# Kernel tuning notes

Hardware: AMD Instinct MI355X
Metric: run time of the kernel (lower is better)

Reference implementation:

```python
import jax, jax.numpy as jnp
import numpy as np

B, N, E = 128, 2048, 32768   # events, nodes per history graph, temporal edges per graph
C, TC, H = 4, 4, 2           # channels, time_channels, heads (hardcoded in source)
DH = C // H
L = 2                        # num_layers


def setup_inputs() -> dict:
    key = jax.random.key(0)
    ks = jax.random.split(key, 16)
    return {
        "x": jax.random.normal(ks[0], (B, N, C), jnp.float32),
        "edge_index": jax.random.randint(ks[1], (B, 2, E), 0, N),
        "edge_time": jax.random.uniform(ks[2], (B, E), jnp.float32),
        "timestamp": jax.random.uniform(ks[3], (B,), jnp.float32),
        "src_index": jax.random.randint(ks[4], (B,), 0, N),
        "dst_index": jax.random.randint(ks[5], (B,), 0, N),
        "time_w": jax.random.normal(ks[6], (TC,), jnp.float32),
        "time_b": jax.random.normal(ks[7], (TC,), jnp.float32),
        "Wq": jax.random.normal(ks[8], (L, C, C), jnp.float32) / np.sqrt(C).astype(np.float32),
        "Wk": jax.random.normal(ks[9], (L, C + TC, C), jnp.float32) / np.sqrt(C + TC).astype(np.float32),
        "Wv": jax.random.normal(ks[10], (L, C + TC, C), jnp.float32) / np.sqrt(C + TC).astype(np.float32),
        "Wo": jax.random.normal(ks[11], (L, C, C), jnp.float32) / np.sqrt(C).astype(np.float32),
        "bo": jnp.zeros((L, C), jnp.float32),
        "W_lin": jax.random.normal(ks[12], (2 * C + TC, 2), jnp.float32) / np.sqrt(2 * C + TC).astype(np.float32),
        "b_lin": jnp.zeros((2,), jnp.float32),
    }


def _time_enc(t, w, b):
    # TimeEncoder: cos(t * w + b)  (Bochner-style functional time encoding)
    return jnp.cos(t[..., None] * w + b)


def _encode(x, src, dst, phi, Wq, Wk, Wv, Wo, bo):
    # seg id per edge: (batch, dst node) -> flat segment for segment softmax
    seg = (jnp.arange(B, dtype=dst.dtype)[:, None] * N + dst).reshape(-1)  # [B*E]
    h = x
    for l in range(L):
        h_src = jnp.take_along_axis(h, src[:, :, None], axis=1)            # [B,E,C] gather source feats
        msg = jnp.concatenate([h_src, phi], axis=-1)                       # [B,E,C+TC]
        q = (h @ Wq[l]).reshape(B, N, C)                                   # [B,N,C]
        k = (msg @ Wk[l]).reshape(B, E, H, DH)
        v = (msg @ Wv[l]).reshape(B, E, H, DH)
        q_e = jnp.take_along_axis(q, dst[:, :, None], axis=1).reshape(B, E, H, DH)
        logits = (q_e * k).sum(-1) / np.float32(np.sqrt(DH))               # [B,E,H]
        lf = logits.reshape(B * E, H)
        m = jax.ops.segment_max(lf, seg, num_segments=B * N)               # stable softmax max
        p = jnp.exp(lf - m[seg])
        s = jax.ops.segment_sum(p, seg, num_segments=B * N)
        agg = jax.ops.segment_sum(p[:, :, None] * v.reshape(B * E, H, DH), seg, num_segments=B * N)
        attn = (agg / jnp.where(s == 0, 1.0, s)[:, :, None]).reshape(B, N, C)
        h = jax.nn.relu(h + attn @ Wo[l] + bo[l])                          # residual + out-proj + relu
    return h


def reference(x, edge_index, edge_time, timestamp, src_index, dst_index,
              time_w, time_b, Wq, Wk, Wv, Wo, bo, W_lin, b_lin):
    src, dst = edge_index[:, 0, :], edge_index[:, 1, :]
    dt = timestamp[:, None] - edge_time                                    # [B,E] time deltas vs query time
    phi = _time_enc(dt, time_w, time_b)                                    # [B,E,TC]
    h = _encode(x, src, dst, phi, Wq, Wk, Wv, Wo, bo)                      # [B,N,C]
    bidx = jnp.arange(B)
    src_x = h[bidx, src_index]                                             # [B,C]
    dst_x = h[bidx, dst_index]                                             # [B,C]
    time_x = _time_enc(timestamp, time_w, time_b)                          # [B,TC]
    feats = jnp.concatenate([src_x, dst_x, time_x], axis=-1)               # [B,12]
    return feats @ W_lin + b_lin                                           # [B,2]
```

## Files before the change

kernel.cpp:

```cpp
#include <hip/hip_runtime.h>
#include <hip/hip_fp16.h>

namespace {

constexpr int B = 128, N = 2048, E = 32768;
constexpr int LOG2N = 11, LOG2E = 15;
constexpr int QE = 8192;

constexpr size_t OFF_H0  = 0;
constexpr size_t OFF_H1  = 4u * 1024 * 1024;
constexpr size_t OFF_SRT = 8u * 1024 * 1024;
constexpr size_t OFF_SEG = 24u * 1024 * 1024;

__global__ __launch_bounds__(1024) void sort_kernel(const int* __restrict__ edge_index,
                                                    const float* __restrict__ edge_time,
                                                    const float* __restrict__ timestamp,
                                                    unsigned* __restrict__ sorted,
                                                    unsigned* __restrict__ seg) {
  __shared__ int      cnt[N];
  __shared__ int      partial[1024];
  __shared__ unsigned rec[QE];
  int blk = blockIdx.x, b = blk >> 2, q = blk & 3, t = threadIdx.x;
  const int* src_arr = edge_index + ((size_t)(2 * b) << LOG2E) + q * QE;
  const int* dst_arr = edge_index + ((size_t)(2 * b + 1) << LOG2E) + q * QE;
  const float* et    = edge_time + ((size_t)b << LOG2E) + q * QE;
  float ts = timestamp[b];

  cnt[t] = 0; cnt[t + 1024] = 0;
  __syncthreads();

  for (int e = t; e < QE; e += 1024) atomicAdd(&cnt[dst_arr[e]], 1);
  __syncthreads();

  int i0 = 2 * t, i1 = 2 * t + 1;
  int l0 = cnt[i0], l1 = cnt[i1], sum = l0 + l1;
  partial[t] = sum;
  __syncthreads();
  for (int d = 1; d < 1024; d <<= 1) {
    int v = (t >= d) ? partial[t - d] : 0;
    __syncthreads();
    partial[t] += v;
    __syncthreads();
  }
  int run = partial[t] - sum;
  int run2 = run + l0;
  unsigned* sg = seg + (size_t)blk * N;
  sg[i0] = (unsigned)run  | ((unsigned)l0 << 16);
  sg[i1] = (unsigned)run2 | ((unsigned)l1 << 16);
  cnt[i0] = run;
  cnt[i1] = run2;
  __syncthreads();

  for (int e = t; e < QE; e += 1024) {
    int dst = dst_arr[e], src = src_arr[e];
    float dt = ts - et[e];
    unsigned hd = (unsigned)__half_as_ushort(__float2half(dt));
    int pos = atomicAdd(&cnt[dst], 1);
    rec[pos] = (unsigned)src | (hd << 16);
  }
  __syncthreads();

  const uint4* rec4 = (const uint4*)rec;
  uint4* out4 = (uint4*)(sorted + ((size_t)blk << 13));
#pragma unroll
  for (int i = t; i < QE / 4; i += 1024) out4[i] = rec4[i];
}

__global__ __launch_bounds__(256) void layer_kernel(const float4* __restrict__ h_in,
                                                    float4* __restrict__ h_out,
                                                    const unsigned* __restrict__ seg,
                                                    const unsigned* __restrict__ sorted,
                                                    const float* __restrict__ tw,
                                                    const float* __restrict__ tb,
                                                    const float* __restrict__ Wq,
                                                    const float* __restrict__ Wk,
                                                    const float* __restrict__ Wv,
                                                    const float* __restrict__ Wo,
                                                    const float* __restrict__ bo) {
  __shared__ float4 lh[N];
  int blk = blockIdx.x, b = blk >> 3, oct = blk & 7, t = threadIdx.x;

  const float4* hb = h_in + ((size_t)b << LOG2N);
#pragma unroll
  for (int j = 0; j < 8; j++) {
    int idx = j * 256 + t;
    lh[idx] = hb[idx];
  }

  float twf[4], tbf[4], bof[4], wq[16], wof[16], wk[32], wv[32];
#pragma unroll
  for (int j = 0; j < 4; j++) { twf[j] = tw[j]; tbf[j] = tb[j]; bof[j] = bo[j]; }
#pragma unroll
  for (int j = 0; j < 16; j++) { wq[j] = Wq[j]; wof[j] = Wo[j]; }
#pragma unroll
  for (int j = 0; j < 32; j++) { wk[j] = Wk[j]; wv[j] = Wv[j]; }
  __syncthreads();

  int n = (oct << 8) + t;
  float4 hn = lh[n];
  float q0 = hn.x * wq[0] + hn.y * wq[4] + hn.z * wq[8]  + hn.w * wq[12];
  float q1 = hn.x * wq[1] + hn.y * wq[5] + hn.z * wq[9]  + hn.w * wq[13];
  float q2 = hn.x * wq[2] + hn.y * wq[6] + hn.z * wq[10] + hn.w * wq[14];
  float q3 = hn.x * wq[3] + hn.y * wq[7] + hn.z * wq[11] + hn.w * wq[15];
  const float RS2 = 0.70710678118654752f;
  float u0[8], u1[8];
#pragma unroll
  for (int j = 0; j < 8; j++) {
    u0[j] = RS2 * (q0 * wk[j * 4 + 0] + q1 * wk[j * 4 + 1]);
    u1[j] = RS2 * (q2 * wk[j * 4 + 2] + q3 * wk[j * 4 + 3]);
  }

  float m0 = -INFINITY, m1 = -INFINITY;
  float s0 = 0.f, s1 = 0.f, a00 = 0.f, a01 = 0.f, a10 = 0.f, a11 = 0.f;

#pragma unroll
  for (int q = 0; q < 4; ++q) {
    int qblk = (b << 2) + q;
    unsigned sd = seg[(size_t)qblk * N + n];
    int beg = (int)(sd & 0xFFFFu);
    int deg = (int)(sd >> 16);
    const unsigned* srt = sorted + ((size_t)qblk << 13) + beg;
    unsigned rc = (deg > 0) ? srt[0] : 0u;
    for (int j = 0; j < deg; ++j) {
      unsigned rc_next = (j + 1 < deg) ? srt[j + 1] : 0u;
      int src = (int)(rc & 0xFFFFu);
      float dt = __half2float(__ushort_as_half((unsigned short)(rc >> 16)));
      float4 hs = lh[src];
      float p0c = __cosf(dt * twf[0] + tbf[0]);
      float p1c = __cosf(dt * twf[1] + tbf[1]);
      float p2c = __cosf(dt * twf[2] + tbf[2]);
      float p3c = __cosf(dt * twf[3] + tbf[3]);
      float l0 = u0[0] * hs.x + u0[1] * hs.y + u0[2] * hs.z + u0[3] * hs.w
               + u0[4] * p0c + u0[5] * p1c + u0[6] * p2c + u0[7] * p3c;
      float l1 = u1[0] * hs.x + u1[1] * hs.y + u1[2] * hs.z + u1[3] * hs.w
               + u1[4] * p0c + u1[5] * p1c + u1[6] * p2c + u1[7] * p3c;
      float v0 = wv[0] * hs.x + wv[4] * hs.y + wv[8]  * hs.z + wv[12] * hs.w
               + wv[16] * p0c + wv[20] * p1c + wv[24] * p2c + wv[28] * p3c;
      float v1 = wv[1] * hs.x + wv[5] * hs.y + wv[9]  * hs.z + wv[13] * hs.w
               + wv[17] * p0c + wv[21] * p1c + wv[25] * p2c + wv[29] * p3c;
      float v2 = wv[2] * hs.x + wv[6] * hs.y + wv[10] * hs.z + wv[14] * hs.w
               + wv[18] * p0c + wv[22] * p1c + wv[26] * p2c + wv[30] * p3c;
      float v3 = wv[3] * hs.x + wv[7] * hs.y + wv[11] * hs.z + wv[15] * hs.w
               + wv[19] * p0c + wv[23] * p1c + wv[27] * p2c + wv[31] * p3c;
      float nm0 = fmaxf(m0, l0);
      float sc0 = __expf(m0 - nm0);
      float p0  = __expf(l0 - nm0);
      s0 = s0 * sc0 + p0; a00 = a00 * sc0 + p0 * v0; a01 = a01 * sc0 + p0 * v1; m0 = nm0;
      float nm1 = fmaxf(m1, l1);
      float sc1 = __expf(m1 - nm1);
      float p1  = __expf(l1 - nm1);
      s1 = s1 * sc1 + p1; a10 = a10 * sc1 + p1 * v2; a11 = a11 * sc1 + p1 * v3; m1 = nm1;
      rc = rc_next;
    }
  }
  float d0 = (s0 == 0.f) ? 1.f : s0;
  float d1 = (s1 == 0.f) ? 1.f : s1;
  float at0 = a00 / d0, at1 = a01 / d0, at2 = a10 / d1, at3 = a11 / d1;
  float o0 = bof[0] + at0 * wof[0] + at1 * wof[4] + at2 * wof[8]  + at3 * wof[12];
  float o1 = bof[1] + at0 * wof[1] + at1 * wof[5] + at2 * wof[9]  + at3 * wof[13];
  float o2 = bof[2] + at0 * wof[2] + at1 * wof[6] + at2 * wof[10] + at3 * wof[14];
  float o3 = bof[3] + at0 * wof[3] + at1 * wof[7] + at2 * wof[11] + at3 * wof[15];
  h_out[((size_t)b << LOG2N) + n] =
      make_float4(fmaxf(hn.x + o0, 0.f), fmaxf(hn.y + o1, 0.f),
                  fmaxf(hn.z + o2, 0.f), fmaxf(hn.w + o3, 0.f));
}

__global__ void final_kernel(const float4* __restrict__ h,
                             const int* __restrict__ src_index, const int* __restrict__ dst_index,
                             const float* __restrict__ timestamp,
                             const float* __restrict__ tw,
                             const float* __restrict__ tb,
                             const float* __restrict__ W_lin,
                             const float* __restrict__ b_lin,
                             float* __restrict__ out) {
  int b = threadIdx.x;
  if (b >= B) return;
  float4 sx = h[(((size_t)b) << LOG2N) + src_index[b]];
  float4 dx = h[(((size_t)b) << LOG2N) + dst_index[b]];
  float ts = timestamp[b];
  float f[12];
  f[0] = sx.x; f[1] = sx.y; f[2] = sx.z; f[3] = sx.w;
  f[4] = dx.x; f[5] = dx.y; f[6] = dx.z; f[7] = dx.w;
#pragma unroll
  for (int j = 0; j < 4; j++) f[8 + j] = __cosf(ts * tw[j] + tb[j]);
#pragma unroll
  for (int c = 0; c < 2; c++) {
    float o = b_lin[c];
#pragma unroll
    for (int j = 0; j < 12; j++) o += f[j] * W_lin[j * 2 + c];
    out[b * 2 + c] = o;
  }
}

}

extern "C" void kernel_launch(void* const* d_in, const int* in_sizes, int n_in,
                              void* d_out, int out_size, void* d_ws, size_t ws_size,
                              hipStream_t stream) {
  (void)in_sizes; (void)n_in; (void)out_size; (void)ws_size;
  const float* x         = (const float*)d_in[0];
  const int*   edge_idx  = (const int*)d_in[1];
  const float* edge_time = (const float*)d_in[2];
  const float* timestamp = (const float*)d_in[3];
  const int*   src_index = (const int*)d_in[4];
  const int*   dst_index = (const int*)d_in[5];
  const float* time_w    = (const float*)d_in[6];
  const float* time_b    = (const float*)d_in[7];
  const float* Wq        = (const float*)d_in[8];
  const float* Wk        = (const float*)d_in[9];
  const float* Wv        = (const float*)d_in[10];
  const float* Wo        = (const float*)d_in[11];
  const float* bo        = (const float*)d_in[12];
  const float* W_lin     = (const float*)d_in[13];
  const float* b_lin     = (const float*)d_in[14];

  char* ws = (char*)d_ws;
  float4*   h0     = (float4*)(ws + OFF_H0);
  float4*   h1     = (float4*)(ws + OFF_H1);
  unsigned* sorted = (unsigned*)(ws + OFF_SRT);
  unsigned* seg    = (unsigned*)(ws + OFF_SEG);

  sort_kernel<<<4 * B, 1024, 0, stream>>>(edge_idx, edge_time, timestamp, sorted, seg);

  layer_kernel<<<8 * B, 256, 0, stream>>>((const float4*)x, h1, seg, sorted,
                                          time_w, time_b,
                                          Wq + 0 * 16, Wk + 0 * 32, Wv + 0 * 32,
                                          Wo + 0 * 16, bo + 0 * 4);
  layer_kernel<<<8 * B, 256, 0, stream>>>(h1, h0, seg, sorted,
                                          time_w, time_b,
                                          Wq + 1 * 16, Wk + 1 * 32, Wv + 1 * 32,
                                          Wo + 1 * 16, bo + 1 * 4);

  final_kernel<<<1, 128, 0, stream>>>(h0, src_index, dst_index, timestamp, time_w, time_b,
                                      W_lin, b_lin, (float*)d_out);
}
```

Baseline: 195.8 us.

## Pad per-node edge lists to multiples of four and process edges in uint4 chunks

The sort kernel now pads each destination node's record segment to a multiple of four, so every segment is 16-byte aligned and the sorted buffer stride grows. The layer kernel loads four packed edge records per uint4 and processes them as a block, using a single online-softmax rescale per chunk instead of one per edge. This targets per-edge scalar global loads and the serial exp/max dependency chain. In exchange it adds wasted work on padded lanes, a larger sorted buffer, and more register pressure from the unrolled four-edge body.

```diff
diff --git a/kernel.cpp b/kernel.cpp
--- a/kernel.cpp
+++ b/kernel.cpp
@@ -6,11 +6,13 @@
 constexpr int B = 128, N = 2048, E = 32768;
 constexpr int LOG2N = 11, LOG2E = 15;
 constexpr int QE = 8192;
+constexpr int RECCAP = 14336;
+constexpr int SSTR = 16384;
 
 constexpr size_t OFF_H0  = 0;
 constexpr size_t OFF_H1  = 4u * 1024 * 1024;
 constexpr size_t OFF_SRT = 8u * 1024 * 1024;
-constexpr size_t OFF_SEG = 24u * 1024 * 1024;
+constexpr size_t OFF_SEG = 40u * 1024 * 1024;
 
 __global__ __launch_bounds__(1024) void sort_kernel(const int* __restrict__ edge_index,
                                                     const float* __restrict__ edge_time,
@@ -19,7 +21,8 @@
                                                     unsigned* __restrict__ seg) {
   __shared__ int      cnt[N];
   __shared__ int      partial[1024];
-  __shared__ unsigned rec[QE];
+  __shared__ int      tot_s;
+  __shared__ unsigned rec[RECCAP];
   int blk = blockIdx.x, b = blk >> 2, q = blk & 3, t = threadIdx.x;
   const int* src_arr = edge_index + ((size_t)(2 * b) << LOG2E) + q * QE;
   const int* dst_arr = edge_index + ((size_t)(2 * b + 1) << LOG2E) + q * QE;
@@ -33,7 +36,9 @@
   __syncthreads();
 
   int i0 = 2 * t, i1 = 2 * t + 1;
-  int l0 = cnt[i0], l1 = cnt[i1], sum = l0 + l1;
+  int d0 = cnt[i0], d1 = cnt[i1];
+  int w0 = (d0 + 3) & ~3, w1 = (d1 + 3) & ~3;
+  int sum = w0 + w1;
   partial[t] = sum;
   __syncthreads();
   for (int d = 1; d < 1024; d <<= 1) {
@@ -43,10 +48,11 @@
     __syncthreads();
   }
   int run = partial[t] - sum;
-  int run2 = run + l0;
+  int run2 = run + w0;
+  if (t == 1023) tot_s = partial[t];
   unsigned* sg = seg + (size_t)blk * N;
-  sg[i0] = (unsigned)run  | ((unsigned)l0 << 16);
-  sg[i1] = (unsigned)run2 | ((unsigned)l1 << 16);
+  sg[i0] = (unsigned)run  | ((unsigned)d0 << 16);
+  sg[i1] = (unsigned)run2 | ((unsigned)d1 << 16);
   cnt[i0] = run;
   cnt[i1] = run2;
   __syncthreads();
@@ -60,10 +66,10 @@
   }
   __syncthreads();
 
+  int tot4 = tot_s >> 2;
   const uint4* rec4 = (const uint4*)rec;
-  uint4* out4 = (uint4*)(sorted + ((size_t)blk << 13));
-#pragma unroll
-  for (int i = t; i < QE / 4; i += 1024) out4[i] = rec4[i];
+  uint4* out4 = (uint4*)(sorted + (size_t)blk * SSTR);
+  for (int i = t; i < tot4; i += 1024) out4[i] = rec4[i];
 }
 
 __global__ __launch_bounds__(256) void layer_kernel(const float4* __restrict__ h_in,
@@ -110,47 +116,80 @@
     u1[j] = RS2 * (q2 * wk[j * 4 + 2] + q3 * wk[j * 4 + 3]);
   }
 
-  float m0 = -INFINITY, m1 = -INFINITY;
-  float s0 = 0.f, s1 = 0.f, a00 = 0.f, a01 = 0.f, a10 = 0.f, a11 = 0.f;
-
+  int begq[4], degq[4];
+  const uint4* sp[4];
 #pragma unroll
   for (int q = 0; q < 4; ++q) {
     int qblk = (b << 2) + q;
     unsigned sd = seg[(size_t)qblk * N + n];
-    int beg = (int)(sd & 0xFFFFu);
-    int deg = (int)(sd >> 16);
-    const unsigned* srt = sorted + ((size_t)qblk << 13) + beg;
-    unsigned rc = (deg > 0) ? srt[0] : 0u;
-    for (int j = 0; j < deg; ++j) {
-      unsigned rc_next = (j + 1 < deg) ? srt[j + 1] : 0u;
-      int src = (int)(rc & 0xFFFFu);
-      float dt = __half2float(__ushort_as_half((unsigned short)(rc >> 16)));
-      float4 hs = lh[src];
-      float p0c = __cosf(dt * twf[0] + tbf[0]);
-      float p1c = __cosf(dt * twf[1] + tbf[1]);
-      float p2c = __cosf(dt * twf[2] + tbf[2]);
-      float p3c = __cosf(dt * twf[3] + tbf[3]);
-      float l0 = u0[0] * hs.x + u0[1] * hs.y + u0[2] * hs.z + u0[3] * hs.w
-               + u0[4] * p0c + u0[5] * p1c + u0[6] * p2c + u0[7] * p3c;
-      float l1 = u1[0] * hs.x + u1[1] * hs.y + u1[2] * hs.z + u1[3] * hs.w
-               + u1[4] * p0c + u1[5] * p1c + u1[6] * p2c + u1[7] * p3c;
-      float v0 = wv[0] * hs.x + wv[4] * hs.y + wv[8]  * hs.z + wv[12] * hs.w
+    begq[q] = (int)(sd & 0xFFFFu);
+    degq[q] = (int)(sd >> 16);
+    sp[q] = (const uint4*)(sorted + (size_t)qblk * SSTR + begq[q]);
+  }
+  uint4 pf[4];
+#pragma unroll
+  for (int q = 0; q < 4; ++q)
+    pf[q] = (degq[q] > 0) ? sp[q][0] : make_uint4(0, 0, 0, 0);
+
+  float m0 = -INFINITY, m1 = -INFINITY;
+  float s0 = 0.f, s1 = 0.f, a00 = 0.f, a01 = 0.f, a10 = 0.f, a11 = 0.f;
+
+#pragma unroll
+  for (int q = 0; q < 4; ++q) {
+    int dg = degq[q];
+    if (dg <= 0) continue;
+    int nch = (dg + 3) >> 2;
+    uint4 cur = pf[q];
+    for (int c = 0; c < nch; ++c) {
+      uint4 nxt = (c + 1 < nch) ? sp[q][c + 1] : make_uint4(0, 0, 0, 0);
+      unsigned rcs[4] = {cur.x, cur.y, cur.z, cur.w};
+      int jb = c << 2;
+      float l0e[4], l1e[4], v0e[4], v1e[4], v2e[4], v3e[4];
+#pragma unroll
+      for (int i = 0; i < 4; ++i) {
+        bool valid = (jb + i) < dg;
+        unsigned rcv = valid ? rcs[i] : 0u;
+        int src = (int)(rcv & 0x7FFu);
+        float dt = __half2float(__ushort_as_half((unsigned short)(rcv >> 16)));
+        float4 hs = lh[src];
+        float p0c = __cosf(dt * twf[0] + tbf[0]);
+        float p1c = __cosf(dt * twf[1] + tbf[1]);
+        float p2c = __cosf(dt * twf[2] + tbf[2]);
+        float p3c = __cosf(dt * twf[3] + tbf[3]);
+        float l0 = u0[0] * hs.x + u0[1] * hs.y + u0[2] * hs.z + u0[3] * hs.w
+                 + u0[4] * p0c + u0[5] * p1c + u0[6] * p2c + u0[7] * p3c;
+        float l1 = u1[0] * hs.x + u1[1] * hs.y + u1[2] * hs.z + u1[3] * hs.w
+                 + u1[4] * p0c + u1[5] * p1c + u1[6] * p2c + u1[7] * p3c;
+        l0e[i] = valid ? l0 : -INFINITY;
+        l1e[i] = valid ? l1 : -INFINITY;
+        v0e[i] = wv[0] * hs.x + wv[4] * hs.y + wv[8]  * hs.z + wv[12] * hs.w
                + wv[16] * p0c + wv[20] * p1c + wv[24] * p2c + wv[28] * p3c;
-      float v1 = wv[1] * hs.x + wv[5] * hs.y + wv[9]  * hs.z + wv[13] * hs.w
+        v1e[i] = wv[1] * hs.x + wv[5] * hs.y + wv[9]  * hs.z + wv[13] * hs.w
                + wv[17] * p0c + wv[21] * p1c + wv[25] * p2c + wv[29] * p3c;
-      float v2 = wv[2] * hs.x + wv[6] * hs.y + wv[10] * hs.z + wv[14] * hs.w
+        v2e[i] = wv[2] * hs.x + wv[6] * hs.y + wv[10] * hs.z + wv[14] * hs.w
                + wv[18] * p0c + wv[22] * p1c + wv[26] * p2c + wv[30] * p3c;
-      float v3 = wv[3] * hs.x + wv[7] * hs.y + wv[11] * hs.z + wv[15] * hs.w
+        v3e[i] = wv[3] * hs.x + wv[7] * hs.y + wv[11] * hs.z + wv[15] * hs.w
                + wv[19] * p0c + wv[23] * p1c + wv[27] * p2c + wv[31] * p3c;
-      float nm0 = fmaxf(m0, l0);
+      }
+      float lx0 = fmaxf(fmaxf(l0e[0], l0e[1]), fmaxf(l0e[2], l0e[3]));
+      float nm0 = fmaxf(m0, lx0);
       float sc0 = __expf(m0 - nm0);
-      float p0  = __expf(l0 - nm0);
-      s0 = s0 * sc0 + p0; a00 = a00 * sc0 + p0 * v0; a01 = a01 * sc0 + p0 * v1; m0 = nm0;
-      float nm1 = fmaxf(m1, l1);
+      float pe0 = __expf(l0e[0] - nm0), pe1 = __expf(l0e[1] - nm0);
+      float pe2 = __expf(l0e[2] - nm0), pe3 = __expf(l0e[3] - nm0);
+      s0  = s0  * sc0 + (pe0 + pe1 + pe2 + pe3);
+      a00 = a00 * sc0 + (pe0 * v0e[0] + pe1 * v0e[1] + pe2 * v0e[2] + pe3 * v0e[3]);
+      a01 = a01 * sc0 + (pe0 * v1e[0] + pe1 * v1e[1] + pe2 * v1e[2] + pe3 * v1e[3]);
+      m0 = nm0;
+      float lx1 = fmaxf(fmaxf(l1e[0], l1e[1]), fmaxf(l1e[2], l1e[3]));
+      float nm1 = fmaxf(m1, lx1);
       float sc1 = __expf(m1 - nm1);
-      float p1  = __expf(l1 - nm1);
-      s1 = s1 * sc1 + p1; a10 = a10 * sc1 + p1 * v2; a11 = a11 * sc1 + p1 * v3; m1 = nm1;
-      rc = rc_next;
+      float qe0 = __expf(l1e[0] - nm1), qe1 = __expf(l1e[1] - nm1);
+      float qe2 = __expf(l1e[2] - nm1), qe3 = __expf(l1e[3] - nm1);
+      s1  = s1  * sc1 + (qe0 + qe1 + qe2 + qe3);
+      a10 = a10 * sc1 + (qe0 * v2e[0] + qe1 * v2e[1] + qe2 * v2e[2] + qe3 * v2e[3]);
+      a11 = a11 * sc1 + (qe0 * v3e[0] + qe1 * v3e[1] + qe2 * v3e[2] + qe3 * v3e[3]);
+      m1 = nm1;
+      cur = nxt;
     }
   }
   float d0 = (s0 == 0.f) ? 1.f : s0;
```

After: 202.5 us. 1.03x slower.
